# Kernel optimization log

Measured on AMD Instinct MI355X. Metric: run time of the kernel, lower is better.

Reference implementation:

```python
import jax, jax.numpy as jnp
import numpy as np

# irrep multiplicities: 32x0e + 16x1o + 16x1e + 8x0o  -> feature size 32+48+48+8 = 136
M0E, M1O, M1E, M0O = 32, 16, 16, 8
FEAT = M0E + 3 * M1O + 3 * M1E + M0O  # 136
WS = {'0e': (M0E + M1O, M0E), '1o': (M0E + M1O + M1E, M1O), '1e': (M1O + M1E + M0O, M1E), '0o': (M1E + M0O, M0O)}
WNUM = sum(a * b for a, b in WS.values())  # 3392
N_NODES, N_EDGES, EDGE_FEAT, HIDDEN = 8192, 65536, 64, 64


def setup_inputs() -> dict:
    key = jax.random.key(0)
    ks = jax.random.split(key, 8)
    return {
        'node_attr': jax.random.normal(ks[0], (N_NODES, FEAT), jnp.float32),
        'edge_index': jax.random.randint(ks[1], (2, N_EDGES), 0, N_NODES),
        'edge_attr': jax.random.normal(ks[2], (N_EDGES, EDGE_FEAT), jnp.float32),
        'edge_sh': jax.random.normal(ks[3], (N_EDGES, 4), jnp.float32),
        'fc_w1': jax.random.normal(ks[4], (EDGE_FEAT, HIDDEN), jnp.float32) / np.sqrt(EDGE_FEAT),
        'fc_b1': jnp.zeros((HIDDEN,), jnp.float32),
        'fc_w2': jax.random.normal(ks[5], (HIDDEN, WNUM), jnp.float32) / np.sqrt(HIDDEN),
        'fc_b2': jnp.zeros((WNUM,), jnp.float32),
    }


def reference(node_attr, edge_index, edge_attr, edge_sh, fc_w1, fc_b1, fc_w2, fc_b2):
    N = node_attr.shape[0]
    src, dst = edge_index[0], edge_index[1]
    # per-edge tensor-product weights via 2-layer MLP (FCBlock, relu)
    w = jax.nn.relu(edge_attr @ fc_w1 + fc_b1) @ fc_w2 + fc_b2  # [E, WNUM]
    x = node_attr[dst]                                          # gather [E, 136]
    x0e = x[:, :M0E]
    x1o = x[:, M0E:M0E + 3 * M1O].reshape(-1, M1O, 3)
    x1e = x[:, M0E + 3 * M1O:M0E + 3 * M1O + 3 * M1E].reshape(-1, M1E, 3)
    x0o = x[:, -M0O:]
    sh0, sh1 = edge_sh[:, 0], edge_sh[:, 1:4]
    inv_s3, inv_s2 = 1.0 / np.sqrt(3.0), 1.0 / np.sqrt(2.0)
    # uncoupled tensor-product outputs per output irrep
    o0e = jnp.concatenate([x0e * sh0[:, None],
                           (x1o * sh1[:, None, :]).sum(-1) * inv_s3], axis=-1)           # [E,48]
    o1o = jnp.concatenate([x0e[:, :, None] * sh1[:, None, :],
                           x1o * sh0[:, None, None],
                           jnp.cross(x1e, sh1[:, None, :]) * inv_s2], axis=1)            # [E,64,3]
    o1e = jnp.concatenate([jnp.cross(x1o, sh1[:, None, :]) * inv_s2,
                           x1e * sh0[:, None, None],
                           x0o[:, :, None] * sh1[:, None, :]], axis=1)                   # [E,40,3]
    o0o = jnp.concatenate([(x1e * sh1[:, None, :]).sum(-1) * inv_s3,
                           x0o * sh0[:, None]], axis=-1)                                 # [E,24]
    # per-edge weight slices, normalized by sqrt(fan_in)
    off = 0
    wd = {}
    for k in ('0e', '1o', '1e', '0o'):
        i, o = WS[k]
        wd[k] = w[:, off:off + i * o].reshape(-1, i, o) / np.sqrt(i)
        off += i * o
    y0e = jnp.einsum('ei,eio->eo', o0e, wd['0e'])
    y1o = jnp.einsum('eic,eio->eoc', o1o, wd['1o']).reshape(-1, 3 * M1O)
    y1e = jnp.einsum('eic,eio->eoc', o1e, wd['1e']).reshape(-1, 3 * M1E)
    y0o = jnp.einsum('ei,eio->eo', o0o, wd['0o'])
    tp = jnp.concatenate([y0e, y1o, y1e, y0o], axis=-1)  # [E,136]
    # scatter-mean to source nodes
    summed = jax.ops.segment_sum(tp, src, num_segments=N)
    cnt = jax.ops.segment_sum(jnp.ones((tp.shape[0],), tp.dtype), src, num_segments=N)
    out = summed / jnp.maximum(cnt, 1.0)[:, None]
    # residual (out_irreps == in_irreps, so no padding needed)
    return out + node_attr
```

## Files before the change

kernel.cpp:

```cpp
#include <hip/hip_runtime.h>

#define N_NODES 8192
#define N_EDGES 65536
#define FEAT    136
#define WNUM    3392

typedef __attribute__((ext_vector_type(4))) short s16x4;
typedef __attribute__((ext_vector_type(8))) short s16x8;
typedef __attribute__((ext_vector_type(4))) float f32x4;
typedef __attribute__((ext_vector_type(2))) float f32x2;

__device__ __forceinline__ float b2f(unsigned short h) {
    union { unsigned int u; float f; } v; v.u = ((unsigned int)h) << 16; return v.f;
}
__device__ __forceinline__ unsigned short f2b(float f) {
    union { float f; unsigned int u; } v; v.f = f;
    unsigned int u = v.u;
    unsigned int r = (u + 0x7FFFu + ((u >> 16) & 1u)) >> 16;
    return (unsigned short)r;
}

__device__ __forceinline__ float wscale(int col) {
    const float inv_s3 = 0.57735026918962576f;
    const float inv_s2 = 0.70710678118654752f;
    if (col < 1536) { int i = col >> 5;          return 0.14433756729740643f * (i < 32 ? 1.f : inv_s3); }
    if (col < 2560) { int i = (col - 1536) >> 4; return 0.125f               * (i >= 48 ? inv_s2 : 1.f); }
    if (col < 3200) { int i = (col - 2560) >> 4; return 0.15811388300841897f * (i < 16 ? inv_s2 : 1.f); }
    {               int i = (col - 3200) >> 3;   return 0.20412414523193150f * (i < 16 ? inv_s3 : 1.f); }
}

__global__ void transpose_kernel(const float* __restrict__ w2,
                                 const float* __restrict__ w1,
                                 const float* __restrict__ bias2,
                                 unsigned short* __restrict__ w2t,
                                 unsigned short* __restrict__ w1t,
                                 float* __restrict__ b2s,
                                 float* __restrict__ zero_base) {
    __shared__ float tl[64 * 65];
    const int b = blockIdx.x, tid = threadIdx.x;
    if (b >= 54) {
        int idx = (b - 54) * 256 + tid;
        float4 z = {0.f, 0.f, 0.f, 0.f};
        if (idx < 280576) ((float4*)zero_base)[idx] = z;
        return;
    }
    if (b < 53) {
        const int c0 = b * 64;
        for (int idx = tid; idx < 4096; idx += 256) {
            int k = idx >> 6, c = idx & 63;
            tl[c * 65 + k] = w2[k * WNUM + c0 + c];
        }
        __syncthreads();
        for (int idx = tid; idx < 4096; idx += 256) {
            int fl   = idx >> 10;
            int rem  = idx & 1023;
            int half = rem >> 9;
            int ln   = (rem >> 3) & 63;
            int j    = idx & 7;
            int q = ln >> 4, nn = ln & 15;
            int cl  = fl * 16 + nn;
            int k   = half * 32 + q * 8 + j;
            int col = c0 + cl;
            w2t[(size_t)b * 4096 + idx] = f2b(tl[cl * 65 + k] * wscale(col));
        }
        if (tid < 64) {
            int col = c0 + tid;
            b2s[col] = bias2[col] * wscale(col);
        }
    } else {
        for (int idx = tid; idx < 4096; idx += 256) {
            int k = idx >> 6, j = idx & 63;
            tl[j * 65 + k] = w1[k * 64 + j];
        }
        __syncthreads();
        for (int idx = tid; idx < 4096; idx += 256) {
            int j = idx >> 6, k = idx & 63;
            w1t[j * 64 + k] = f2b(tl[j * 65 + k]);
        }
    }
}

__device__ __forceinline__ void gload_lds16(const unsigned short* g, unsigned short* l) {
    __builtin_amdgcn_global_load_lds(
        (const __attribute__((address_space(1))) unsigned int*)g,
        (__attribute__((address_space(3))) unsigned int*)l, 16, 0, 0);
}

__global__ __launch_bounds__(256, 4)
void tpconv_main(const float* __restrict__ node_attr,
                 const int* __restrict__ edge_index,
                 const float* __restrict__ edge_attr,
                 const float* __restrict__ edge_sh,
                 const unsigned short* __restrict__ w1t,
                 const float* __restrict__ b1,
                 const unsigned short* __restrict__ w2t,
                 const float* __restrict__ b2s,
                 float* __restrict__ acc_g,
                 float* __restrict__ cnt_g) {
    __shared__ __align__(16) char smem[37632];
    unsigned short* x_lds = (unsigned short*)smem;
    unsigned short* wbuf  = (unsigned short*)(smem + 18944);
    unsigned short* h_lds = (unsigned short*)(smem + 18944);
    float* sh_lds = (float*)(smem + 28160);
    int* dst_lds  = (int*)(smem + 29184);
    int* src_lds  = (int*)(smem + 37120);

    const int tid  = threadIdx.x;
    const int lane = tid & 63;
    const int wv   = tid >> 6;
    const int n    = lane & 15;
    const int quad = lane >> 4;
    const int eb   = blockIdx.x * 64;

    if (tid < 64) {
        int s = edge_index[eb + tid];
        int d = edge_index[N_EDGES + eb + tid];
        src_lds[tid] = s;
        dst_lds[tid] = d;
        atomicAdd(&cnt_g[s], 1.0f);
        const float4 shv = *(const float4*)&edge_sh[(size_t)(eb + tid) * 4];
        sh_lds[tid * 4 + 0] = shv.x;
        sh_lds[tid * 4 + 1] = shv.y;
        sh_lds[tid * 4 + 2] = shv.z;
        sh_lds[tid * 4 + 3] = shv.w;
    }
    {
        const float* ea = edge_attr + (size_t)(eb + wv * 16 + n) * 64 + quad * 8;
        s16x8 a0, a1;
#pragma unroll
        for (int j = 0; j < 8; ++j) {
            a0[j] = (short)f2b(ea[j]);
            a1[j] = (short)f2b(ea[32 + j]);
        }
        for (int ct = 0; ct < 4; ++ct) {
            int col = ct * 16 + n;
            const unsigned short* wp = w1t + col * 64;
            s16x8 bu0 = *(const s16x8*)&wp[quad * 8];
            s16x8 bu1 = *(const s16x8*)&wp[32 + quad * 8];
            f32x4 acc = {0.f, 0.f, 0.f, 0.f};
            acc = __builtin_amdgcn_mfma_f32_16x16x32_bf16(a0, bu0, acc, 0, 0, 0);
            acc = __builtin_amdgcn_mfma_f32_16x16x32_bf16(a1, bu1, acc, 0, 0, 0);
            float bias = b1[col];
            for (int r = 0; r < 4; ++r) {
                float hv = acc[r] + bias;
                hv = hv > 0.f ? hv : 0.f;
                h_lds[(wv * 16 + quad * 4 + r) * 72 + col] = f2b(hv);
            }
        }
    }
    __syncthreads();

    for (int idx = tid; idx < 64 * 34; idx += 256) {
        int e = idx / 34, seg = idx - e * 34;
        const float4 v = *(const float4*)(node_attr + (size_t)dst_lds[e] * FEAT + seg * 4);
        s16x4 pk;
        pk[0] = (short)f2b(v.x); pk[1] = (short)f2b(v.y);
        pk[2] = (short)f2b(v.z); pk[3] = (short)f2b(v.w);
        *(s16x4*)&x_lds[e * 148 + seg * 4] = pk;
    }
    const int eLoc = wv * 16 + n;
    const float sh0 = sh_lds[eLoc * 4 + 0];
    const float s1x = sh_lds[eLoc * 4 + 1];
    const float s1y = sh_lds[eLoc * 4 + 2];
    const float s1z = sh_lds[eLoc * 4 + 3];
    const unsigned short* hp = &h_lds[eLoc * 72];
    s16x8 h0 = *(const s16x8*)&hp[quad * 8];
    s16x8 h1 = *(const s16x8*)&hp[32 + quad * 8];
    const unsigned short* xr = &x_lds[eLoc * 148];

    __syncthreads();

    {
        const unsigned short* g = w2t + (wv << 10) + (lane << 3);
        unsigned short* l = wbuf + (wv << 10);
        gload_lds16(g, l);
        gload_lds16(g + 512, l + 512);
    }

    f32x2 Y0e2[2][2] = {};
    f32x2 Y1o2[2][3] = {};
    f32x2 Y1e2[2][3] = {};
    f32x2 Y0o2[2]    = {};

#define CHUNK_TOP(c)                                                          \
    __syncthreads();                                                          \
    if ((c) < 52) {                                                           \
        const unsigned short* g = w2t + (((size_t)(c) + 1) << 12) + (wv << 10) + (lane << 3); \
        unsigned short* l = wbuf + ((((c) + 1) & 1) << 12) + (wv << 10);      \
        gload_lds16(g, l);                                                    \
        gload_lds16(g + 512, l + 512);                                        \
    }                                                                         \
    f32x4 bvv[4];                                                             \
    _Pragma("unroll")                                                         \
    for (int t = 0; t < 4; ++t)                                               \
        bvv[t] = *(const f32x4*)(b2s + (c) * 64 + 16 * t + quad * 4);         \
    const unsigned short* cb = wbuf + (((c) & 1) << 12);

#define MFMA_T(t)                                                             \
    s16x8 aT0 = *(const s16x8*)&cb[(t) * 1024 + (lane << 3)];                 \
    s16x8 aT1 = *(const s16x8*)&cb[(t) * 1024 + 512 + (lane << 3)];           \
    f32x4 acc = bvv[t];                                                       \
    acc = __builtin_amdgcn_mfma_f32_16x16x32_bf16(aT0, h0, acc, 0, 0, 0);     \
    acc = __builtin_amdgcn_mfma_f32_16x16x32_bf16(aT1, h1, acc, 0, 0, 0);     \
    f32x2 a01 = {acc[0], acc[1]}; f32x2 a23 = {acc[2], acc[3]};

#define ACC3(Y)                                                               \
    Y[0][0] += a01 * o0; Y[1][0] += a23 * o0;                                 \
    Y[0][1] += a01 * o1; Y[1][1] += a23 * o1;                                 \
    Y[0][2] += a01 * o2; Y[1][2] += a23 * o2;

    for (int c = 0; c < 16; ++c) {
        CHUNK_TOP(c)
        float ov = 0.f;
#pragma unroll
        for (int t = 0; t < 4; ++t) {
            MFMA_T(t)
            if ((t & 1) == 0) ov = b2f(xr[2 * c + (t >> 1)]) * sh0;
            const int kk = t & 1;
            Y0e2[0][kk] += a01 * ov;
            Y0e2[1][kk] += a23 * ov;
        }
    }
    for (int c = 16; c < 24; ++c) {
        CHUNK_TOP(c)
        float ov = 0.f;
#pragma unroll
        for (int t = 0; t < 4; ++t) {
            MFMA_T(t)
            if ((t & 1) == 0) {
                int ib = 32 + 3 * (2 * c + (t >> 1) - 32);
                ov = b2f(xr[ib]) * s1x + b2f(xr[ib + 1]) * s1y + b2f(xr[ib + 2]) * s1z;
            }
            const int kk = t & 1;
            Y0e2[0][kk] += a01 * ov;
            Y0e2[1][kk] += a23 * ov;
        }
    }
    for (int c = 24; c < 32; ++c) {
        CHUNK_TOP(c)
#pragma unroll
        for (int t = 0; t < 4; ++t) {
            MFMA_T(t)
            float xv = b2f(xr[4 * (c - 24) + t]);
            float o0 = xv * s1x, o1 = xv * s1y, o2 = xv * s1z;
            ACC3(Y1o2)
        }
    }
    for (int c = 32; c < 36; ++c) {
        CHUNK_TOP(c)
#pragma unroll
        for (int t = 0; t < 4; ++t) {
            MFMA_T(t)
            int ib = 32 + 3 * (4 * (c - 24) + t - 32);
            float o0 = b2f(xr[ib]) * sh0, o1 = b2f(xr[ib + 1]) * sh0, o2 = b2f(xr[ib + 2]) * sh0;
            ACC3(Y1o2)
        }
    }
    for (int c = 36; c < 40; ++c) {
        CHUNK_TOP(c)
#pragma unroll
        for (int t = 0; t < 4; ++t) {
            MFMA_T(t)
            int ib = 80 + 3 * (4 * (c - 24) + t - 48);
            float av0 = b2f(xr[ib]), av1 = b2f(xr[ib + 1]), av2 = b2f(xr[ib + 2]);
            float o0 = av1 * s1z - av2 * s1y;
            float o1 = av2 * s1x - av0 * s1z;
            float o2 = av0 * s1y - av1 * s1x;
            ACC3(Y1o2)
        }
    }
    for (int c = 40; c < 44; ++c) {
        CHUNK_TOP(c)
#pragma unroll
        for (int t = 0; t < 4; ++t) {
            MFMA_T(t)
            int ib = 32 + 3 * (4 * (c - 40) + t);
            float av0 = b2f(xr[ib]), av1 = b2f(xr[ib + 1]), av2 = b2f(xr[ib + 2]);
            float o0 = av1 * s1z - av2 * s1y;
            float o1 = av2 * s1x - av0 * s1z;
            float o2 = av0 * s1y - av1 * s1x;
            ACC3(Y1e2)
        }
    }
    for (int c = 44; c < 48; ++c) {
        CHUNK_TOP(c)
#pragma unroll
        for (int t = 0; t < 4; ++t) {
            MFMA_T(t)
            int ib = 80 + 3 * (4 * (c - 40) + t - 16);
            float o0 = b2f(xr[ib]) * sh0, o1 = b2f(xr[ib + 1]) * sh0, o2 = b2f(xr[ib + 2]) * sh0;
            ACC3(Y1e2)
        }
    }
    for (int c = 48; c < 50; ++c) {
        CHUNK_TOP(c)
#pragma unroll
        for (int t = 0; t < 4; ++t) {
            MFMA_T(t)
            float xv = b2f(xr[128 + (4 * (c - 40) + t - 32)]);
            float o0 = xv * s1x, o1 = xv * s1y, o2 = xv * s1z;
            ACC3(Y1e2)
        }
    }
    for (int c = 50; c < 52; ++c) {
        CHUNK_TOP(c)
#pragma unroll
        for (int t = 0; t < 4; ++t) {
            MFMA_T(t)
            int ib = 80 + 3 * (8 * (c - 50) + 2 * t + (quad >> 1));
            float ov = b2f(xr[ib]) * s1x + b2f(xr[ib + 1]) * s1y + b2f(xr[ib + 2]) * s1z;
            Y0o2[0] += a01 * ov;
            Y0o2[1] += a23 * ov;
        }
    }
    {
        CHUNK_TOP(52)
#pragma unroll
        for (int t = 0; t < 4; ++t) {
            MFMA_T(t)
            float ov = b2f(xr[128 + 2 * t + (quad >> 1)]) * sh0;
            Y0o2[0] += a01 * ov;
            Y0o2[1] += a23 * ov;
        }
    }
#undef ACC3
#undef MFMA_T
#undef CHUNK_TOP

    __syncthreads();
    float* stage = (float*)smem;
    {
        float* srow = stage + eLoc * 145;
#pragma unroll
        for (int r = 0; r < 4; ++r) {
            const int p = r >> 1, s = r & 1;
            int qr = quad * 4 + r;
            srow[qr]              = Y0e2[p][0][s];
            srow[16 + qr]         = Y0e2[p][1][s];
            srow[32 + qr * 3 + 0] = Y1o2[p][0][s];
            srow[32 + qr * 3 + 1] = Y1o2[p][1][s];
            srow[32 + qr * 3 + 2] = Y1o2[p][2][s];
            srow[80 + qr * 3 + 0] = Y1e2[p][0][s];
            srow[80 + qr * 3 + 1] = Y1e2[p][1][s];
            srow[80 + qr * 3 + 2] = Y1e2[p][2][s];
            srow[128 + (quad & 1) * 4 + r + (quad >> 1) * 8] = Y0o2[p][s];
        }
    }
    __syncthreads();
    for (int j = 0; j < 16; ++j) {
        int e = wv * 16 + j;
        float* dp = acc_g + (size_t)src_lds[e] * FEAT;
        const float* sr = stage + e * 145;
        atomicAdd(dp + lane,      sr[lane]);
        atomicAdd(dp + 64 + lane, sr[64 + lane]);
        if (lane < 8)
            atomicAdd(dp + 128 + lane, sr[128 + lane] + sr[136 + lane]);
    }
}

__global__ void finalize_kernel(const float* __restrict__ acc_g,
                                const float* __restrict__ cnt_g,
                                const float* __restrict__ node_attr,
                                float* __restrict__ out) {
    int idx = blockIdx.x * 256 + threadIdx.x;
    if (idx >= N_NODES * FEAT) return;
    int nn = idx / FEAT;
    float c = cnt_g[nn];
    out[idx] = acc_g[idx] / fmaxf(c, 1.0f) + node_attr[idx];
}

extern "C" void kernel_launch(void* const* d_in, const int* in_sizes, int n_in,
                              void* d_out, int out_size, void* d_ws, size_t ws_size,
                              hipStream_t stream) {
    const float* node_attr  = (const float*)d_in[0];
    const int*   edge_index = (const int*)d_in[1];
    const float* edge_attr  = (const float*)d_in[2];
    const float* edge_sh    = (const float*)d_in[3];
    const float* fc_w1      = (const float*)d_in[4];
    const float* fc_b1      = (const float*)d_in[5];
    const float* fc_w2      = (const float*)d_in[6];
    const float* fc_b2      = (const float*)d_in[7];
    float* out = (float*)d_out;

    char* ws = (char*)d_ws;
    float* acc_g = (float*)ws;
    float* cnt_g = (float*)(ws + 4456448);
    unsigned short* w2t = (unsigned short*)(ws + 4489216);
    unsigned short* w1t = (unsigned short*)(ws + 4489216 + 434176);
    float* b2s = (float*)(ws + 4489216 + 434176 + 8192);

    transpose_kernel<<<1150, 256, 0, stream>>>(fc_w2, fc_w1, fc_b2, w2t, w1t, b2s, acc_g);
    tpconv_main<<<1024, 256, 0, stream>>>(node_attr, edge_index, edge_attr, edge_sh,
                                          w1t, fc_b1, w2t, b2s, acc_g, cnt_g);
    finalize_kernel<<<(N_NODES * FEAT + 255) / 256, 256, 0, stream>>>(acc_g, cnt_g, node_attr, out);
}
```

Before: 164.8 us.

## Switch per-edge weight GEMM to 32x32x16 MFMA with column/edge wave split

Replaces the 16x16x32 bf16 MFMA tiling with 32x32x16 MFMAs. Each wave now covers 32 edges by 32 weight columns, with waves split into column-half and edge-half groups. The packed w2 layout in the prep kernel is reordered to match the new A-operand fragment layout. The per-edge tensor-product accumulation is re-indexed for the new accumulator layout, and the two column-half partial sums are combined through LDS in two phases before the atomic scatter. The aim is fewer MFMA issues and LDS fragment loads per chunk. In exchange it uses larger accumulator register tiles and adds an extra LDS staging pass.

Result: slower. 174.5 us (+5.9%).

```diff
diff --git a/kernel.cpp b/kernel.cpp
--- a/kernel.cpp
+++ b/kernel.cpp
@@ -9,6 +9,7 @@
 typedef __attribute__((ext_vector_type(8))) short s16x8;
 typedef __attribute__((ext_vector_type(4))) float f32x4;
 typedef __attribute__((ext_vector_type(2))) float f32x2;
+typedef __attribute__((ext_vector_type(16))) float f32x16;
 
 __device__ __forceinline__ float b2f(unsigned short h) {
     union { unsigned int u; float f; } v; v.u = ((unsigned int)h) << 16; return v.f;
@@ -52,14 +53,12 @@
         }
         __syncthreads();
         for (int idx = tid; idx < 4096; idx += 256) {
-            int fl   = idx >> 10;
-            int rem  = idx & 1023;
-            int half = rem >> 9;
-            int ln   = (rem >> 3) & 63;
-            int j    = idx & 7;
-            int q = ln >> 4, nn = ln & 15;
-            int cl  = fl * 16 + nn;
-            int k   = half * 32 + q * 8 + j;
+            int tc  = idx >> 11;
+            int ks  = (idx >> 9) & 3;
+            int l   = (idx >> 3) & 63;
+            int j   = idx & 7;
+            int k   = ks * 16 + (l >> 5) * 8 + j;
+            int cl  = tc * 32 + (l & 31);
             int col = c0 + cl;
             w2t[(size_t)b * 4096 + idx] = f2b(tl[cl * 65 + k] * wscale(col));
         }
@@ -110,6 +109,10 @@
     const int wv   = tid >> 6;
     const int n    = lane & 15;
     const int quad = lane >> 4;
+    const int m31  = lane & 31;
+    const int hi   = lane >> 5;
+    const int tc   = wv >> 1;
+    const int et   = wv & 1;
     const int eb   = blockIdx.x * 64;
 
     if (tid < 64) {
@@ -158,203 +161,229 @@
         pk[2] = (short)f2b(v.z); pk[3] = (short)f2b(v.w);
         *(s16x4*)&x_lds[e * 148 + seg * 4] = pk;
     }
-    const int eLoc = wv * 16 + n;
-    const float sh0 = sh_lds[eLoc * 4 + 0];
-    const float s1x = sh_lds[eLoc * 4 + 1];
-    const float s1y = sh_lds[eLoc * 4 + 2];
-    const float s1z = sh_lds[eLoc * 4 + 3];
-    const unsigned short* hp = &h_lds[eLoc * 72];
-    s16x8 h0 = *(const s16x8*)&hp[quad * 8];
-    s16x8 h1 = *(const s16x8*)&hp[32 + quad * 8];
-    const unsigned short* xr = &x_lds[eLoc * 148];
+    const int edge = et * 32 + m31;
+    const float sh0 = sh_lds[edge * 4 + 0];
+    const float s1x = sh_lds[edge * 4 + 1];
+    const float s1y = sh_lds[edge * 4 + 2];
+    const float s1z = sh_lds[edge * 4 + 3];
+    s16x8 hf[4];
+#pragma unroll
+    for (int ks = 0; ks < 4; ++ks)
+        hf[ks] = *(const s16x8*)&h_lds[edge * 72 + ks * 16 + hi * 8];
+    const unsigned short* xr = &x_lds[edge * 148];
 
     __syncthreads();
 
     {
-        const unsigned short* g = w2t + (wv << 10) + (lane << 3);
-        unsigned short* l = wbuf + (wv << 10);
-        gload_lds16(g, l);
-        gload_lds16(g + 512, l + 512);
-    }
-
-    f32x2 Y0e2[2][2] = {};
-    f32x2 Y1o2[2][3] = {};
-    f32x2 Y1e2[2][3] = {};
+        const unsigned short* gp = w2t + (wv << 10) + (lane << 3);
+        unsigned short* lp = wbuf + (wv << 10);
+        gload_lds16(gp, lp);
+        gload_lds16(gp + 512, lp + 512);
+    }
+
+    f32x2 Y0e2[8]    = {};
+    f32x2 Y1o2[4][3] = {};
+    f32x2 Y1e2[4][3] = {};
     f32x2 Y0o2[2]    = {};
 
-#define CHUNK_TOP(c)                                                          \
+#define CHUNK_GEMM(c)                                                         \
     __syncthreads();                                                          \
     if ((c) < 52) {                                                           \
-        const unsigned short* g = w2t + (((size_t)(c) + 1) << 12) + (wv << 10) + (lane << 3); \
-        unsigned short* l = wbuf + ((((c) + 1) & 1) << 12) + (wv << 10);      \
-        gload_lds16(g, l);                                                    \
-        gload_lds16(g + 512, l + 512);                                        \
+        const unsigned short* gp = w2t + (((size_t)(c) + 1) << 12) + (wv << 10) + (lane << 3); \
+        unsigned short* lp = wbuf + ((((c) + 1) & 1) << 12) + (wv << 10);     \
+        gload_lds16(gp, lp);                                                  \
+        gload_lds16(gp + 512, lp + 512);                                      \
     }                                                                         \
-    f32x4 bvv[4];                                                             \
+    f32x16 acc;                                                               \
+    {                                                                         \
+        const float* bb = b2s + (c) * 64 + tc * 32 + 4 * hi;                  \
+        _Pragma("unroll")                                                     \
+        for (int g2 = 0; g2 < 4; ++g2) {                                      \
+            f32x4 bv = *(const f32x4*)(bb + 8 * g2);                          \
+            acc[4 * g2 + 0] = bv[0]; acc[4 * g2 + 1] = bv[1];                 \
+            acc[4 * g2 + 2] = bv[2]; acc[4 * g2 + 3] = bv[3];                 \
+        }                                                                     \
+    }                                                                         \
+    {                                                                         \
+        const unsigned short* cb = wbuf + (((c) & 1) << 12) + tc * 2048 + (lane << 3); \
+        _Pragma("unroll")                                                     \
+        for (int ks = 0; ks < 4; ++ks) {                                      \
+            s16x8 av = *(const s16x8*)(cb + ks * 512);                        \
+            acc = __builtin_amdgcn_mfma_f32_32x32x16_bf16(av, hf[ks], acc, 0, 0, 0); \
+        }                                                                     \
+    }
+
+#define UPD0E                                                                 \
     _Pragma("unroll")                                                         \
-    for (int t = 0; t < 4; ++t)                                               \
-        bvv[t] = *(const f32x4*)(b2s + (c) * 64 + 16 * t + quad * 4);         \
-    const unsigned short* cb = wbuf + (((c) & 1) << 12);
-
-#define MFMA_T(t)                                                             \
-    s16x8 aT0 = *(const s16x8*)&cb[(t) * 1024 + (lane << 3)];                 \
-    s16x8 aT1 = *(const s16x8*)&cb[(t) * 1024 + 512 + (lane << 3)];           \
-    f32x4 acc = bvv[t];                                                       \
-    acc = __builtin_amdgcn_mfma_f32_16x16x32_bf16(aT0, h0, acc, 0, 0, 0);     \
-    acc = __builtin_amdgcn_mfma_f32_16x16x32_bf16(aT1, h1, acc, 0, 0, 0);     \
-    f32x2 a01 = {acc[0], acc[1]}; f32x2 a23 = {acc[2], acc[3]};
-
-#define ACC3(Y)                                                               \
-    Y[0][0] += a01 * o0; Y[1][0] += a23 * o0;                                 \
-    Y[0][1] += a01 * o1; Y[1][1] += a23 * o1;                                 \
-    Y[0][2] += a01 * o2; Y[1][2] += a23 * o2;
+    for (int p = 0; p < 8; ++p) {                                             \
+        f32x2 ap = {acc[2 * p], acc[2 * p + 1]};                              \
+        Y0e2[p] += ap * ov;                                                   \
+    }
+
+#define UPD12(Y)                                                              \
+    _Pragma("unroll")                                                         \
+    for (int b = 0; b < 2; ++b) {                                             \
+        _Pragma("unroll")                                                     \
+        for (int q = 0; q < 4; ++q) {                                         \
+            f32x2 ap = {acc[8 * b + 2 * q], acc[8 * b + 2 * q + 1]};          \
+            Y[q][0] += ap * o0[b];                                            \
+            Y[q][1] += ap * o1[b];                                            \
+            Y[q][2] += ap * o2[b];                                            \
+        }                                                                     \
+    }
 
     for (int c = 0; c < 16; ++c) {
-        CHUNK_TOP(c)
-        float ov = 0.f;
-#pragma unroll
-        for (int t = 0; t < 4; ++t) {
-            MFMA_T(t)
-            if ((t & 1) == 0) ov = b2f(xr[2 * c + (t >> 1)]) * sh0;
-            const int kk = t & 1;
-            Y0e2[0][kk] += a01 * ov;
-            Y0e2[1][kk] += a23 * ov;
-        }
+        CHUNK_GEMM(c)
+        const float ov = b2f(xr[2 * c + tc]) * sh0;
+        UPD0E
     }
     for (int c = 16; c < 24; ++c) {
-        CHUNK_TOP(c)
-        float ov = 0.f;
-#pragma unroll
-        for (int t = 0; t < 4; ++t) {
-            MFMA_T(t)
-            if ((t & 1) == 0) {
-                int ib = 32 + 3 * (2 * c + (t >> 1) - 32);
-                ov = b2f(xr[ib]) * s1x + b2f(xr[ib + 1]) * s1y + b2f(xr[ib + 2]) * s1z;
-            }
-            const int kk = t & 1;
-            Y0e2[0][kk] += a01 * ov;
-            Y0e2[1][kk] += a23 * ov;
-        }
+        CHUNK_GEMM(c)
+        int ib = 32 + 3 * (2 * c + tc - 32);
+        const float ov = b2f(xr[ib]) * s1x + b2f(xr[ib + 1]) * s1y + b2f(xr[ib + 2]) * s1z;
+        UPD0E
     }
     for (int c = 24; c < 32; ++c) {
-        CHUNK_TOP(c)
-#pragma unroll
-        for (int t = 0; t < 4; ++t) {
-            MFMA_T(t)
-            float xv = b2f(xr[4 * (c - 24) + t]);
-            float o0 = xv * s1x, o1 = xv * s1y, o2 = xv * s1z;
-            ACC3(Y1o2)
-        }
+        CHUNK_GEMM(c)
+        const int i0 = 4 * (c - 24) + 2 * tc;
+        float o0[2], o1[2], o2[2];
+#pragma unroll
+        for (int b = 0; b < 2; ++b) {
+            float xv = b2f(xr[i0 + b]);
+            o0[b] = xv * s1x; o1[b] = xv * s1y; o2[b] = xv * s1z;
+        }
+        UPD12(Y1o2)
     }
     for (int c = 32; c < 36; ++c) {
-        CHUNK_TOP(c)
-#pragma unroll
-        for (int t = 0; t < 4; ++t) {
-            MFMA_T(t)
-            int ib = 32 + 3 * (4 * (c - 24) + t - 32);
-            float o0 = b2f(xr[ib]) * sh0, o1 = b2f(xr[ib + 1]) * sh0, o2 = b2f(xr[ib + 2]) * sh0;
-            ACC3(Y1o2)
-        }
+        CHUNK_GEMM(c)
+        const int i0 = 4 * (c - 24) + 2 * tc;
+        float o0[2], o1[2], o2[2];
+#pragma unroll
+        for (int b = 0; b < 2; ++b) {
+            int ib = 32 + 3 * (i0 + b - 32);
+            o0[b] = b2f(xr[ib]) * sh0; o1[b] = b2f(xr[ib + 1]) * sh0; o2[b] = b2f(xr[ib + 2]) * sh0;
+        }
+        UPD12(Y1o2)
     }
     for (int c = 36; c < 40; ++c) {
-        CHUNK_TOP(c)
-#pragma unroll
-        for (int t = 0; t < 4; ++t) {
-            MFMA_T(t)
-            int ib = 80 + 3 * (4 * (c - 24) + t - 48);
-            float av0 = b2f(xr[ib]), av1 = b2f(xr[ib + 1]), av2 = b2f(xr[ib + 2]);
-            float o0 = av1 * s1z - av2 * s1y;
-            float o1 = av2 * s1x - av0 * s1z;
-            float o2 = av0 * s1y - av1 * s1x;
-            ACC3(Y1o2)
-        }
+        CHUNK_GEMM(c)
+        const int i0 = 4 * (c - 24) + 2 * tc;
+        float o0[2], o1[2], o2[2];
+#pragma unroll
+        for (int b = 0; b < 2; ++b) {
+            int ib = 80 + 3 * (i0 + b - 48);
+            float a0v = b2f(xr[ib]), a1v = b2f(xr[ib + 1]), a2v = b2f(xr[ib + 2]);
+            o0[b] = a1v * s1z - a2v * s1y;
+            o1[b] = a2v * s1x - a0v * s1z;
+            o2[b] = a0v * s1y - a1v * s1x;
+        }
+        UPD12(Y1o2)
     }
     for (int c = 40; c < 44; ++c) {
-        CHUNK_TOP(c)
-#pragma unroll
-        for (int t = 0; t < 4; ++t) {
-            MFMA_T(t)
-            int ib = 32 + 3 * (4 * (c - 40) + t);
-            float av0 = b2f(xr[ib]), av1 = b2f(xr[ib + 1]), av2 = b2f(xr[ib + 2]);
-            float o0 = av1 * s1z - av2 * s1y;
-            float o1 = av2 * s1x - av0 * s1z;
-            float o2 = av0 * s1y - av1 * s1x;
-            ACC3(Y1e2)
-        }
+        CHUNK_GEMM(c)
+        const int i0 = 4 * (c - 40) + 2 * tc;
+        float o0[2], o1[2], o2[2];
+#pragma unroll
+        for (int b = 0; b < 2; ++b) {
+            int ib = 32 + 3 * (i0 + b);
+            float a0v = b2f(xr[ib]), a1v = b2f(xr[ib + 1]), a2v = b2f(xr[ib + 2]);
+            o0[b] = a1v * s1z - a2v * s1y;
+            o1[b] = a2v * s1x - a0v * s1z;
+            o2[b] = a0v * s1y - a1v * s1x;
+        }
+        UPD12(Y1e2)
     }
     for (int c = 44; c < 48; ++c) {
-        CHUNK_TOP(c)
-#pragma unroll
-        for (int t = 0; t < 4; ++t) {
-            MFMA_T(t)
-            int ib = 80 + 3 * (4 * (c - 40) + t - 16);
-            float o0 = b2f(xr[ib]) * sh0, o1 = b2f(xr[ib + 1]) * sh0, o2 = b2f(xr[ib + 2]) * sh0;
-            ACC3(Y1e2)
-        }
+        CHUNK_GEMM(c)
+        const int i0 = 4 * (c - 40) + 2 * tc;
+        float o0[2], o1[2], o2[2];
+#pragma unroll
+        for (int b = 0; b < 2; ++b) {
+            int ib = 80 + 3 * (i0 + b - 16);
+            o0[b] = b2f(xr[ib]) * sh0; o1[b] = b2f(xr[ib + 1]) * sh0; o2[b] = b2f(xr[ib + 2]) * sh0;
+        }
+        UPD12(Y1e2)
     }
     for (int c = 48; c < 50; ++c) {
-        CHUNK_TOP(c)
-#pragma unroll
-        for (int t = 0; t < 4; ++t) {
-            MFMA_T(t)
-            float xv = b2f(xr[128 + (4 * (c - 40) + t - 32)]);
-            float o0 = xv * s1x, o1 = xv * s1y, o2 = xv * s1z;
-            ACC3(Y1e2)
-        }
+        CHUNK_GEMM(c)
+        const int i0 = 4 * (c - 40) + 2 * tc;
+        float o0[2], o1[2], o2[2];
+#pragma unroll
+        for (int b = 0; b < 2; ++b) {
+            float xv = b2f(xr[128 + (i0 + b - 32)]);
+            o0[b] = xv * s1x; o1[b] = xv * s1y; o2[b] = xv * s1z;
+        }
+        UPD12(Y1e2)
     }
     for (int c = 50; c < 52; ++c) {
-        CHUNK_TOP(c)
-#pragma unroll
-        for (int t = 0; t < 4; ++t) {
-            MFMA_T(t)
-            int ib = 80 + 3 * (8 * (c - 50) + 2 * t + (quad >> 1));
+        CHUNK_GEMM(c)
+#pragma unroll
+        for (int g = 0; g < 4; ++g) {
+            int ib = 80 + 3 * (8 * (c - 50) + 4 * tc + g);
             float ov = b2f(xr[ib]) * s1x + b2f(xr[ib + 1]) * s1y + b2f(xr[ib + 2]) * s1z;
+            f32x2 a01 = {acc[4 * g], acc[4 * g + 1]};
+            f32x2 a23 = {acc[4 * g + 2], acc[4 * g + 3]};
             Y0o2[0] += a01 * ov;
             Y0o2[1] += a23 * ov;
         }
     }
     {
-        CHUNK_TOP(52)
-#pragma unroll
-        for (int t = 0; t < 4; ++t) {
-            MFMA_T(t)
-            float ov = b2f(xr[128 + 2 * t + (quad >> 1)]) * sh0;
+        CHUNK_GEMM(52)
+#pragma unroll
+        for (int g = 0; g < 4; ++g) {
+            float ov = b2f(xr[128 + 4 * tc + g]) * sh0;
+            f32x2 a01 = {acc[4 * g], acc[4 * g + 1]};
+            f32x2 a23 = {acc[4 * g + 2], acc[4 * g + 3]};
             Y0o2[0] += a01 * ov;
             Y0o2[1] += a23 * ov;
         }
     }
-#undef ACC3
-#undef MFMA_T
-#undef CHUNK_TOP
+#undef CHUNK_GEMM
+#undef UPD0E
+#undef UPD12
 
     __syncthreads();
     float* stage = (float*)smem;
-    {
-        float* srow = stage + eLoc * 145;
-#pragma unroll
-        for (int r = 0; r < 4; ++r) {
-            const int p = r >> 1, s = r & 1;
-            int qr = quad * 4 + r;
-            srow[qr]              = Y0e2[p][0][s];
-            srow[16 + qr]         = Y0e2[p][1][s];
-            srow[32 + qr * 3 + 0] = Y1o2[p][0][s];
-            srow[32 + qr * 3 + 1] = Y1o2[p][1][s];
-            srow[32 + qr * 3 + 2] = Y1o2[p][2][s];
-            srow[80 + qr * 3 + 0] = Y1e2[p][0][s];
-            srow[80 + qr * 3 + 1] = Y1e2[p][1][s];
-            srow[80 + qr * 3 + 2] = Y1e2[p][2][s];
-            srow[128 + (quad & 1) * 4 + r + (quad >> 1) * 8] = Y0o2[p][s];
-        }
-    }
+    float* srow = stage + (size_t)edge * 145;
+    const int h4 = 4 * hi;
+
+#define EMIT(OPEQ)                                                            \
+    _Pragma("unroll")                                                         \
+    for (int p = 0; p < 8; ++p) {                                             \
+        int ob = (p & 1) * 2 + ((p >> 1) & 1) * 8 + (p >> 2) * 16 + h4;       \
+        srow[ob]     OPEQ Y0e2[p][0];                                         \
+        srow[ob + 1] OPEQ Y0e2[p][1];                                         \
+    }                                                                         \
+    _Pragma("unroll")                                                         \
+    for (int q = 0; q < 4; ++q) {                                             \
+        int ob = (q & 1) * 2 + (q >> 1) * 8 + h4;                             \
+        _Pragma("unroll")                                                     \
+        for (int m = 0; m < 3; ++m) {                                         \
+            srow[32 + ob * 3 + m]       OPEQ Y1o2[q][m][0];                   \
+            srow[32 + (ob + 1) * 3 + m] OPEQ Y1o2[q][m][1];                   \
+            srow[80 + ob * 3 + m]       OPEQ Y1e2[q][m][0];                   \
+            srow[80 + (ob + 1) * 3 + m] OPEQ Y1e2[q][m][1];                   \
+        }                                                                     \
+    }                                                                         \
+    srow[128 + h4]     OPEQ Y0o2[0][0];                                       \
+    srow[128 + h4 + 1] OPEQ Y0o2[0][1];                                       \
+    srow[128 + h4 + 2] OPEQ Y0o2[1][0];                                       \
+    srow[128 + h4 + 3] OPEQ Y0o2[1][1];
+
+    if (tc == 0) { EMIT(=) }
     __syncthreads();
+    if (tc == 1) { EMIT(+=) }
+#undef EMIT
+    __syncthreads();
+
     for (int j = 0; j < 16; ++j) {
         int e = wv * 16 + j;
         float* dp = acc_g + (size_t)src_lds[e] * FEAT;
-        const float* sr = stage + e * 145;
+        const float* sr = stage + (size_t)e * 145;
         atomicAdd(dp + lane,      sr[lane]);
         atomicAdd(dp + 64 + lane, sr[64 + lane]);
         if (lane < 8)
-            atomicAdd(dp + 128 + lane, sr[128 + lane] + sr[136 + lane]);
+            atomicAdd(dp + 128 + lane, sr[128 + lane]);
     }
 }
 
```
